# Performance work log

Measured on AMD Instinct MI355X. Metric: run time of the kernel, lower is better.

## Reference

```python
import jax, jax.numpy as jnp
import numpy as np

THRESH = 1.0        # cif_weight_threshold
MAX_HIST = 10       # max_history
RELU_THRESH = 1.0   # relu_threshold (crelu clip)
NORM_SCALAR = 1.0   # normalize_scalar


def setup_inputs() -> dict:
    key = jax.random.key(0)
    k0, k1, k2 = jax.random.split(key, 3)
    B, T, H = 32, 2048, 256
    encoder_outputs = jax.random.normal(k0, (B, T, H), jnp.float32)
    mask = jnp.ones((B, 200, 1), jnp.float32)
    W1 = jax.random.normal(k1, (2 * H, 2 * H), jnp.float32) * 0.02
    b1 = jnp.zeros((2 * H,), jnp.float32)
    W2 = jax.random.normal(k2, (1, 2 * H), jnp.float32) * 0.02
    b2 = jnp.zeros((1,), jnp.float32)
    return {"encoder_outputs": encoder_outputs, "mask": mask,
            "W1": W1, "b1": b1, "W2": W2, "b2": b2, "is_training": 1}


def _cif_forward(x, mask, W1, b1, W2, b2, is_training):
    B, T, H = x.shape
    dt = x.dtype
    # number of non-zero (effective) frames per utterance
    first_pad = jnp.sum((jnp.sum(jnp.abs(x), -1) != 0.0).astype(jnp.int32), 1)  # [B]

    # ---- history chunk: mean over window [max(0, t-MAX_HIST), t); t==0 uses x[:,0] ----
    cs = jnp.concatenate([jnp.zeros((B, 1, H), dt), jnp.cumsum(x, axis=1)], axis=1)  # [B,T+1,H]
    t_idx = jnp.arange(T)
    start = jnp.maximum(0, t_idx - MAX_HIST)
    count = jnp.maximum(t_idx - start, 1).astype(dt)
    hist = (cs[:, t_idx, :] - cs[:, start, :]) / count[None, :, None]     # [B,T,H]
    hist = jnp.where((t_idx == 0)[None, :, None], x[:, 0:1, :], hist)

    # ---- weight prediction (two dense layers, crelu + clip) ----
    info = jnp.concatenate([x, x - hist], axis=-1)                        # [B,T,2H]
    h = jnp.einsum('btc,oc->bto', info, W1) + b1
    w = (jnp.einsum('btc,oc->bto', h, W2) + b2)[..., 0]                   # [B,T]
    w = jnp.clip(jax.nn.relu(w), None, RELU_THRESH)
    ori_weight = w
    sum_a = w.sum(1)

    if is_training:  # static python int; using_scaling=True, mask provided
        N = mask[:, :, 0].sum(-1) - 1.0
        scale = N / jnp.clip(sum_a, 1e-8)
        scale = jnp.where(sum_a == 0, jnp.zeros_like(sum_a), scale)
        w = scale[:, None] * w

    pad_mask = t_idx[None, :] > first_pad[:, None]                        # [B,T]
    w = jnp.where(pad_mask, 0.0, w)

    # ---- accumulate-and-fire scan ----
    def step(carry, inp):
        prev_w, prev_s = carry
        w_t, x_t = inp                                                    # [B], [B,H]
        fired = prev_w + w_t > THRESH
        remained = THRESH - prev_w
        new_w = jnp.where(fired, w_t - remained, w_t + prev_w)
        integ = prev_s + (1.0 - w_t)[:, None] * x_t
        new_s = jnp.where(fired[:, None], x_t, integ)
        fired_s = jnp.where(fired[:, None], integ, jnp.zeros_like(integ))
        return (new_w, new_s), (fired, fired_s)

    init = (jnp.zeros((B,), dt), x[:, 0, :])
    (fin_w, fin_s), (fired_flags, fired_states) = jax.lax.scan(
        step, init, (w.T, jnp.swapaxes(x, 0, 1)))

    fired_states = jnp.swapaxes(fired_states, 0, 1)                       # [B,T,H]
    fired_flag = fired_flags.T[:, :, None].astype(dt)                     # [B,T,1]
    fired_states = jnp.where(pad_mask[:, :, None], 0.0, fired_states)
    fired_states = jnp.concatenate([fired_states, fin_s[:, None, :]], 1)  # [B,T+1,H] (tail)

    # ---- compact fired states to the front (torch truncates to max fired len;
    #      here we keep fixed length T+1 and pad with zeros, which is a superset) ----
    L = T + 1
    fired_marks = (jnp.sum(jnp.abs(fired_states), -1) != 0.0).astype(jnp.int32)
    pos = jnp.cumsum(fired_marks, axis=1) - 1
    pos = jnp.where(fired_marks == 1, pos, L)  # out-of-bounds -> dropped
    cif = jnp.zeros((B, L, H), dt)
    cif = cif.at[jnp.arange(B)[:, None], pos].set(fired_states, mode='drop')

    not_padding_after_cif = (jnp.sum(jnp.abs(cif), -1) != 0.0).astype(jnp.int32)
    norm = jnp.linalg.norm(cif, axis=-1, keepdims=True)
    cif = NORM_SCALAR * cif / jnp.maximum(norm, 1e-12)  # F.normalize(p=2)
    return cif, ori_weight, fired_flag, not_padding_after_cif, sum_a


def reference(encoder_outputs, mask, W1, b1, W2, b2, is_training):
    return _cif_forward(encoder_outputs, mask, W1, b1, W2, b2, is_training)
```

## Files before the change

kernel.cpp:

```cpp
#include <hip/hip_runtime.h>

#define B_ 32
#define T_ 2048
#define H_ 256
#define L_ 2049

__device__ inline double waveReduceD(double v) {
#pragma unroll
  for (int off = 32; off > 0; off >>= 1) v += __shfl_xor(v, off, 64);
  return v;
}

typedef float vfloat4 __attribute__((ext_vector_type(4)));
__device__ inline void nt_store4(float4 v, float* p) {
  vfloat4 t;
  t.x = v.x; t.y = v.y; t.z = v.z; t.w = v.w;
  __builtin_nontemporal_store(t, (vfloat4*)p);
}

__global__ void __launch_bounds__(256) k0_fold(
    const float* __restrict__ W1, const float* __restrict__ b1,
    const float* __restrict__ W2, const float* __restrict__ b2,
    double* __restrict__ vd, double* __restrict__ c0) {
  __shared__ double s_p[8][32];
  int tid = threadIdx.x;
  int cl = tid & 31, sl = tid >> 5;
  int c = blockIdx.x * 32 + cl;
  double acc0 = 0.0, acc1 = 0.0;
#pragma unroll 4
  for (int o = sl * 64; o < sl * 64 + 64; o += 2) {
    acc0 += (double)W2[o] * (double)W1[o * 512 + c];
    acc1 += (double)W2[o + 1] * (double)W1[(o + 1) * 512 + c];
  }
  s_p[sl][cl] = acc0 + acc1;
  __syncthreads();
  if (sl == 0) {
    double v = 0.0;
#pragma unroll
    for (int i = 0; i < 8; ++i) v += s_p[i][cl];
    vd[c] = v;
  }
  if (blockIdx.x == 0) {
    __shared__ double red[256];
    double p = (double)W2[tid] * (double)b1[tid] +
               (double)W2[tid + 256] * (double)b1[tid + 256];
    red[tid] = p;
    __syncthreads();
    for (int s = 128; s > 0; s >>= 1) {
      if (tid < s) red[tid] += red[tid + s];
      __syncthreads();
    }
    if (tid == 0) c0[0] = red[0] + (double)b2[0];
  }
}

__global__ void __launch_bounds__(256) k1_rowdots(
    const float* __restrict__ x, const double* __restrict__ vd,
    double* __restrict__ d1, double* __restrict__ d2, float* __restrict__ absS) {
  int tid = threadIdx.x;
  int s = tid & 15;
  int slot = tid >> 4;
  long rowBase = (long)blockIdx.x * 64;

  double v12[16], v2v[16];
#pragma unroll
  for (int k = 0; k < 16; ++k) {
    double bv = vd[256 + s * 16 + k];
    v2v[k] = bv;
    v12[k] = vd[s * 16 + k] + bv;
  }

#pragma unroll
  for (int i = 0; i < 4; ++i) {
    long row = rowBase + slot * 4 + i;
    const float4* xr = (const float4*)(x + row * H_ + s * 16);
    float4 a0 = xr[0], a1 = xr[1], a2 = xr[2], a3 = xr[3];
    float e[16];
    *(float4*)(e + 0) = a0; *(float4*)(e + 4) = a1;
    *(float4*)(e + 8) = a2; *(float4*)(e + 12) = a3;
    double p1 = 0.0, p2 = 0.0;
    bool nz = false;
#pragma unroll
    for (int k = 0; k < 16; ++k) {
      p1 += (double)e[k] * v12[k];
      p2 += (double)e[k] * v2v[k];
      nz |= (e[k] != 0.0f);
    }
    float nzf = nz ? 1.0f : 0.0f;
#pragma unroll
    for (int off = 1; off < 16; off <<= 1) {
      p1 += __shfl_xor(p1, off, 64);
      p2 += __shfl_xor(p2, off, 64);
      nzf += __shfl_xor(nzf, off, 64);
    }
    if (s == 0) {
      d1[row] = p1;
      d2[row] = p2;
      absS[row] = (nzf > 0.0f) ? 1.0f : 0.0f;
    }
  }
}

__global__ void __launch_bounds__(256) k2_weights(
    const double* __restrict__ d1, const double* __restrict__ d2,
    const float* __restrict__ absS, const float* __restrict__ mask,
    const int* __restrict__ is_tr, const double* __restrict__ c0p,
    float* __restrict__ o_ori, float* __restrict__ o_sa, float* __restrict__ o_ff,
    float* __restrict__ wsc, int* __restrict__ fireT,
    int* __restrict__ nAllArr, int* __restrict__ nUnmArr) {
  __shared__ double s_P[T_];
  __shared__ double s_tot[4];
  __shared__ double s_red[4][3];
  __shared__ double s_tot2[4];
  __shared__ double s_mtot[4];
  __shared__ int s_int[2];
  int b = blockIdx.x, tid = threadIdx.x;
  int lane = tid & 63, wv = tid >> 6;
  int t0 = tid * 8;
  const double* d1b = d1 + (long)b * T_;
  const double* d2b = d2 + (long)b * T_;
  const float* asb = absS + (long)b * T_;
  double c0 = c0p[0];

  double r2[8];
  {
    double run2 = 0.0;
#pragma unroll
    for (int k = 0; k < 8; ++k) { run2 += d2b[t0 + k]; r2[k] = run2; }
    double sc2 = run2;
#pragma unroll
    for (int off = 1; off < 64; off <<= 1) {
      double n = __shfl_up(sc2, off, 64);
      if (lane >= off) sc2 += n;
    }
    if (lane == 63) s_tot[wv] = sc2;
    __syncthreads();
    double base2 = 0.0;
    for (int i = 0; i < wv; ++i) base2 += s_tot[i];
    double e2 = base2 + (sc2 - run2);
#pragma unroll
    for (int k = 0; k < 8; ++k) s_P[t0 + k] = e2 + r2[k];
  }
  __syncthreads();

  double wd[8];
  double sa = 0.0, fpc = 0.0;
#pragma unroll
  for (int k = 0; k < 8; ++k) {
    int t = t0 + k;
    double wvv;
    if (t == 0) {
      wvv = d1b[0] - s_P[0] + c0;
    } else {
      int start = t - 10; if (start < 0) start = 0;
      double ws_ = s_P[t - 1] - (start > 0 ? s_P[start - 1] : 0.0);
      wvv = d1b[t] - ws_ / (double)(t - start) + c0;
    }
    wvv = wvv < 0.0 ? 0.0 : (wvv > 1.0 ? 1.0 : wvv);
    wd[k] = wvv;
    sa += wvv;
    fpc += (asb[t] != 0.0f) ? 1.0 : 0.0;
  }
  {
    float4* ov = (float4*)(o_ori + (long)b * T_ + t0);
    ov[0] = make_float4((float)wd[0], (float)wd[1], (float)wd[2], (float)wd[3]);
    ov[1] = make_float4((float)wd[4], (float)wd[5], (float)wd[6], (float)wd[7]);
  }
  double ms = (tid < 200) ? (double)mask[(long)b * 200 + tid] : 0.0;
  double sar = waveReduceD(sa), fpr = waveReduceD(fpc), msr = waveReduceD(ms);
  if (lane == 0) { s_red[wv][0] = sar; s_red[wv][1] = fpr; s_red[wv][2] = msr; }
  __syncthreads();
  double sumA = s_red[0][0] + s_red[1][0] + s_red[2][0] + s_red[3][0];
  double fpD  = s_red[0][1] + s_red[1][1] + s_red[2][1] + s_red[3][1];
  double maskSum = s_red[0][2] + s_red[1][2] + s_red[2][2] + s_red[3][2];
  if (tid == 0) o_sa[b] = (float)sumA;
  int firstPad = (int)(fpD + 0.5);
  double scale;
  if (is_tr[0] != 0) {
    scale = (sumA == 0.0) ? 0.0 : (maskSum - 1.0) / (sumA > 1e-8 ? sumA : 1e-8);
  } else {
    scale = 1.0;
  }

  double a[8], r[8];
  double run = 0.0;
#pragma unroll
  for (int k = 0; k < 8; ++k) {
    int t = t0 + k;
    double av = wd[k] * scale;
    if (t > firstPad) av = 0.0;
    a[k] = av;
    run += av; r[k] = run;
  }
  {
    float4* wvv = (float4*)(wsc + (long)b * T_ + t0);
    wvv[0] = make_float4((float)a[0], (float)a[1], (float)a[2], (float)a[3]);
    wvv[1] = make_float4((float)a[4], (float)a[5], (float)a[6], (float)a[7]);
  }
  double sc = run;
#pragma unroll
  for (int off = 1; off < 64; off <<= 1) {
    double n = __shfl_up(sc, off, 64);
    if (lane >= off) sc += n;
  }
  if (lane == 63) s_tot2[wv] = sc;
  __syncthreads();
  double base = 0.0;
  for (int i = 0; i < wv; ++i) base += s_tot2[i];
  double e = base + (sc - run);

  double m[8];
  double mn = 1e300;
#pragma unroll
  for (int k = 0; k < 8; ++k) {
    double S = e + r[k];
    double kp = ceil(S - 1.0); if (kp < 0.0) kp = 0.0;
    double D = kp - (double)(t0 + k);
    mn = fmin(mn, D);
    m[k] = mn;
  }
  double scm = mn;
#pragma unroll
  for (int off = 1; off < 64; off <<= 1) {
    double n = __shfl_up(scm, off, 64);
    if (lane >= off) scm = fmin(scm, n);
  }
  double exw = __shfl_up(scm, 1, 64);
  if (lane == 0) exw = 1e300;
  if (lane == 63) s_mtot[wv] = scm;
  __syncthreads();
  double mbase = 1e300;
  for (int i = 0; i < wv; ++i) mbase = fmin(mbase, s_mtot[i]);
  double Mexcl = fmin(mbase, exw);

  float flags[8];
  int Cp = (t0 - 1) + (int)fmin(1.0, Mexcl);
#pragma unroll
  for (int k = 0; k < 8; ++k) {
    int t = t0 + k;
    double Mk = fmin(Mexcl, m[k]);
    int C = t + (int)fmin(1.0, Mk);
    bool fired = C > Cp;
    flags[k] = fired ? 1.0f : 0.0f;
    if (fired) fireT[(long)b * T_ + (C - 1)] = t;
    if (t == firstPad) s_int[0] = C;
    Cp = C;
  }
  {
    float4* fv = (float4*)(o_ff + (long)b * T_ + t0);
    fv[0] = make_float4(flags[0], flags[1], flags[2], flags[3]);
    fv[1] = make_float4(flags[4], flags[5], flags[6], flags[7]);
  }
  if (tid == 255) s_int[1] = Cp;
  __syncthreads();
  if (tid == 0) {
    int nA = s_int[1];
    nAllArr[b] = nA;
    nUnmArr[b] = (firstPad >= T_) ? nA : s_int[0];
  }
}

__global__ void __launch_bounds__(256) k4_rows(
    const float* __restrict__ x, const float* __restrict__ wsc,
    const int* __restrict__ fireT,
    const int* __restrict__ nAllArr, const int* __restrict__ nUnmArr,
    float* __restrict__ cif, float* __restrict__ notpad) {
  int wave = threadIdx.x >> 6, lane = threadIdx.x & 63;
  int pos = blockIdx.x * 4 + wave;
  int b = blockIdx.y;
  if (pos >= L_) return;
  int nA = nAllArr[b], nU = nUnmArr[b];
  float* crow = cif + ((long)b * L_ + pos) * H_ + lane * 4;
  if (pos > nU) {
    nt_store4(make_float4(0.0f, 0.0f, 0.0f, 0.0f), crow);
    if (lane == 0) notpad[(long)b * L_ + pos] = 0.0f;
    return;
  }
  const int* ftb = fireT + (long)b * T_;
  int hi, anchor, lo;
  if (pos < nU) {
    hi = ftb[pos];
    anchor = (pos == 0) ? 0 : ftb[pos - 1];
    lo = (pos == 0) ? 0 : anchor + 1;
  } else {
    hi = T_ - 1;
    anchor = (nA == 0) ? 0 : ftb[nA - 1];
    lo = (nA == 0) ? 0 : anchor + 1;
  }
  const float* xb = x + (long)b * T_ * H_;
  float4 acc = ((const float4*)(xb + (long)anchor * H_))[lane];
  float4 acc2 = make_float4(0.0f, 0.0f, 0.0f, 0.0f);
  const float* wb = wsc + (long)b * T_;
  int u = lo;
  for (; u + 1 <= hi; u += 2) {
    float f0 = 1.0f - wb[u];
    float f1 = 1.0f - wb[u + 1];
    float4 xv0 = ((const float4*)(xb + (long)u * H_))[lane];
    float4 xv1 = ((const float4*)(xb + (long)(u + 1) * H_))[lane];
    acc.x += f0 * xv0.x;  acc.y += f0 * xv0.y;
    acc.z += f0 * xv0.z;  acc.w += f0 * xv0.w;
    acc2.x += f1 * xv1.x; acc2.y += f1 * xv1.y;
    acc2.z += f1 * xv1.z; acc2.w += f1 * xv1.w;
  }
  if (u <= hi) {
    float f = 1.0f - wb[u];
    float4 xv = ((const float4*)(xb + (long)u * H_))[lane];
    acc.x += f * xv.x; acc.y += f * xv.y; acc.z += f * xv.z; acc.w += f * xv.w;
  }
  acc.x += acc2.x; acc.y += acc2.y; acc.z += acc2.z; acc.w += acc2.w;
  float ss = acc.x * acc.x + acc.y * acc.y + acc.z * acc.z + acc.w * acc.w;
#pragma unroll
  for (int off = 32; off > 0; off >>= 1) ss += __shfl_xor(ss, off, 64);
  float inv = 1.0f / fmaxf(sqrtf(ss), 1e-12f);
  nt_store4(make_float4(acc.x * inv, acc.y * inv, acc.z * inv, acc.w * inv), crow);
  if (lane == 0) notpad[(long)b * L_ + pos] = 1.0f;
}

extern "C" void kernel_launch(void* const* d_in, const int* in_sizes, int n_in,
                              void* d_out, int out_size, void* d_ws, size_t ws_size,
                              hipStream_t stream) {
  const float* x    = (const float*)d_in[0];
  const float* mask = (const float*)d_in[1];
  const float* W1   = (const float*)d_in[2];
  const float* b1   = (const float*)d_in[3];
  const float* W2   = (const float*)d_in[4];
  const float* b2   = (const float*)d_in[5];
  const int*   istr = (const int*)d_in[6];

  float* out = (float*)d_out;
  float* o_cif = out;
  float* o_ori = o_cif + (size_t)B_ * L_ * H_;
  float* o_ff  = o_ori + (size_t)B_ * T_;
  float* o_np  = o_ff  + (size_t)B_ * T_;
  float* o_sa  = o_np  + (size_t)B_ * L_;

  char* w = (char*)d_ws;
  double* vd   = (double*)w; w += 512 * 8;
  double* c0   = (double*)w; w += 8;
  double* d1   = (double*)w; w += (size_t)B_ * T_ * 8;
  double* d2   = (double*)w; w += (size_t)B_ * T_ * 8;
  float* absS  = (float*)w;  w += (size_t)B_ * T_ * 4;
  float* wsc   = (float*)w;  w += (size_t)B_ * T_ * 4;
  int* fireT   = (int*)w;    w += (size_t)B_ * T_ * 4;
  int* nAllA   = (int*)w;    w += B_ * 4;
  int* nUnmA   = (int*)w;    w += B_ * 4;

  k0_fold<<<16, 256, 0, stream>>>(W1, b1, W2, b2, vd, c0);
  k1_rowdots<<<(B_ * T_) / 64, 256, 0, stream>>>(x, vd, d1, d2, absS);
  k2_weights<<<B_, 256, 0, stream>>>(d1, d2, absS, mask, istr, c0,
                                     o_ori, o_sa, o_ff, wsc, fireT,
                                     nAllA, nUnmA);
  k4_rows<<<dim3((L_ + 3) / 4, B_), 256, 0, stream>>>(
      x, wsc, fireT, nAllA, nUnmA, o_cif, o_np);
}
```

Before: 153.1 us.

## Fuse four CIF kernels into one cooperative persistent kernel with grid syncs

```diff
diff --git a/kernel.cpp b/kernel.cpp
--- a/kernel.cpp
+++ b/kernel.cpp
@@ -1,4 +1,7 @@
 #include <hip/hip_runtime.h>
+#include <hip/hip_cooperative_groups.h>
+
+namespace cg = cooperative_groups;
 
 #define B_ 32
 #define T_ 2048
@@ -18,302 +21,307 @@
   __builtin_nontemporal_store(t, (vfloat4*)p);
 }
 
-__global__ void __launch_bounds__(256) k0_fold(
+__global__ void __launch_bounds__(256, 2) cif_fused(
+    const float* __restrict__ x, const float* __restrict__ mask,
     const float* __restrict__ W1, const float* __restrict__ b1,
     const float* __restrict__ W2, const float* __restrict__ b2,
-    double* __restrict__ vd, double* __restrict__ c0) {
-  __shared__ double s_p[8][32];
-  int tid = threadIdx.x;
-  int cl = tid & 31, sl = tid >> 5;
-  int c = blockIdx.x * 32 + cl;
-  double acc0 = 0.0, acc1 = 0.0;
-#pragma unroll 4
-  for (int o = sl * 64; o < sl * 64 + 64; o += 2) {
-    acc0 += (double)W2[o] * (double)W1[o * 512 + c];
-    acc1 += (double)W2[o + 1] * (double)W1[(o + 1) * 512 + c];
-  }
-  s_p[sl][cl] = acc0 + acc1;
-  __syncthreads();
-  if (sl == 0) {
-    double v = 0.0;
-#pragma unroll
-    for (int i = 0; i < 8; ++i) v += s_p[i][cl];
-    vd[c] = v;
-  }
-  if (blockIdx.x == 0) {
-    __shared__ double red[256];
-    double p = (double)W2[tid] * (double)b1[tid] +
-               (double)W2[tid + 256] * (double)b1[tid + 256];
-    red[tid] = p;
-    __syncthreads();
-    for (int s = 128; s > 0; s >>= 1) {
-      if (tid < s) red[tid] += red[tid + s];
-      __syncthreads();
-    }
-    if (tid == 0) c0[0] = red[0] + (double)b2[0];
-  }
-}
-
-__global__ void __launch_bounds__(256) k1_rowdots(
-    const float* __restrict__ x, const double* __restrict__ vd,
-    double* __restrict__ d1, double* __restrict__ d2, float* __restrict__ absS) {
-  int tid = threadIdx.x;
-  int s = tid & 15;
-  int slot = tid >> 4;
-  long rowBase = (long)blockIdx.x * 64;
-
-  double v12[16], v2v[16];
-#pragma unroll
-  for (int k = 0; k < 16; ++k) {
-    double bv = vd[256 + s * 16 + k];
-    v2v[k] = bv;
-    v12[k] = vd[s * 16 + k] + bv;
-  }
-
-#pragma unroll
-  for (int i = 0; i < 4; ++i) {
-    long row = rowBase + slot * 4 + i;
-    const float4* xr = (const float4*)(x + row * H_ + s * 16);
-    float4 a0 = xr[0], a1 = xr[1], a2 = xr[2], a3 = xr[3];
-    float e[16];
-    *(float4*)(e + 0) = a0; *(float4*)(e + 4) = a1;
-    *(float4*)(e + 8) = a2; *(float4*)(e + 12) = a3;
-    double p1 = 0.0, p2 = 0.0;
-    bool nz = false;
-#pragma unroll
-    for (int k = 0; k < 16; ++k) {
-      p1 += (double)e[k] * v12[k];
-      p2 += (double)e[k] * v2v[k];
-      nz |= (e[k] != 0.0f);
-    }
-    float nzf = nz ? 1.0f : 0.0f;
-#pragma unroll
-    for (int off = 1; off < 16; off <<= 1) {
-      p1 += __shfl_xor(p1, off, 64);
-      p2 += __shfl_xor(p2, off, 64);
-      nzf += __shfl_xor(nzf, off, 64);
-    }
-    if (s == 0) {
-      d1[row] = p1;
-      d2[row] = p2;
-      absS[row] = (nzf > 0.0f) ? 1.0f : 0.0f;
-    }
-  }
-}
-
-__global__ void __launch_bounds__(256) k2_weights(
-    const double* __restrict__ d1, const double* __restrict__ d2,
-    const float* __restrict__ absS, const float* __restrict__ mask,
-    const int* __restrict__ is_tr, const double* __restrict__ c0p,
-    float* __restrict__ o_ori, float* __restrict__ o_sa, float* __restrict__ o_ff,
-    float* __restrict__ wsc, int* __restrict__ fireT,
-    int* __restrict__ nAllArr, int* __restrict__ nUnmArr) {
+    const int* __restrict__ is_tr,
+    double* __restrict__ vd, double* __restrict__ c0p,
+    double* __restrict__ d1, double* __restrict__ d2,
+    float* __restrict__ absS, float* __restrict__ wsc,
+    int* __restrict__ fireT, int* __restrict__ nAllArr, int* __restrict__ nUnmArr,
+    float* __restrict__ o_cif, float* __restrict__ o_ori,
+    float* __restrict__ o_ff, float* __restrict__ o_np, float* __restrict__ o_sa) {
+  cg::grid_group grid = cg::this_grid();
   __shared__ double s_P[T_];
   __shared__ double s_tot[4];
   __shared__ double s_red[4][3];
   __shared__ double s_tot2[4];
   __shared__ double s_mtot[4];
   __shared__ int s_int[2];
-  int b = blockIdx.x, tid = threadIdx.x;
-  int lane = tid & 63, wv = tid >> 6;
-  int t0 = tid * 8;
-  const double* d1b = d1 + (long)b * T_;
-  const double* d2b = d2 + (long)b * T_;
-  const float* asb = absS + (long)b * T_;
-  double c0 = c0p[0];
-
-  double r2[8];
+  int tid = threadIdx.x;
+
+  if (blockIdx.x < 16) {
+    double (*s_p)[32] = (double(*)[32])s_P;
+    double* red = s_P + 256;
+    int cl = tid & 31, sl = tid >> 5;
+    int c = blockIdx.x * 32 + cl;
+    double acc0 = 0.0, acc1 = 0.0;
+#pragma unroll 4
+    for (int o = sl * 64; o < sl * 64 + 64; o += 2) {
+      acc0 += (double)W2[o] * (double)W1[o * 512 + c];
+      acc1 += (double)W2[o + 1] * (double)W1[(o + 1) * 512 + c];
+    }
+    s_p[sl][cl] = acc0 + acc1;
+    __syncthreads();
+    if (sl == 0) {
+      double v = 0.0;
+#pragma unroll
+      for (int i = 0; i < 8; ++i) v += s_p[i][cl];
+      vd[c] = v;
+    }
+    if (blockIdx.x == 0) {
+      __syncthreads();
+      red[tid] = (double)W2[tid] * (double)b1[tid] +
+                 (double)W2[tid + 256] * (double)b1[tid + 256];
+      __syncthreads();
+      for (int s = 128; s > 0; s >>= 1) {
+        if (tid < s) red[tid] += red[tid + s];
+        __syncthreads();
+      }
+      if (tid == 0) c0p[0] = red[0] + (double)b2[0];
+    }
+  }
+  grid.sync();
+
   {
-    double run2 = 0.0;
-#pragma unroll
-    for (int k = 0; k < 8; ++k) { run2 += d2b[t0 + k]; r2[k] = run2; }
-    double sc2 = run2;
+    int s = tid & 15;
+    int slot = tid >> 4;
+    double v12[16], v2v[16];
+#pragma unroll
+    for (int k = 0; k < 16; ++k) {
+      double bv = vd[256 + s * 16 + k];
+      v2v[k] = bv;
+      v12[k] = vd[s * 16 + k] + bv;
+    }
+#pragma unroll
+    for (int g = 0; g < 2; ++g) {
+      long rowBase = (long)blockIdx.x * 128 + g * 64;
+#pragma unroll
+      for (int i = 0; i < 4; ++i) {
+        long row = rowBase + slot * 4 + i;
+        const float4* xr = (const float4*)(x + row * H_ + s * 16);
+        float4 a0 = xr[0], a1 = xr[1], a2 = xr[2], a3 = xr[3];
+        float e[16];
+        *(float4*)(e + 0) = a0; *(float4*)(e + 4) = a1;
+        *(float4*)(e + 8) = a2; *(float4*)(e + 12) = a3;
+        double p1 = 0.0, p2 = 0.0;
+        bool nz = false;
+#pragma unroll
+        for (int k = 0; k < 16; ++k) {
+          p1 += (double)e[k] * v12[k];
+          p2 += (double)e[k] * v2v[k];
+          nz |= (e[k] != 0.0f);
+        }
+        float nzf = nz ? 1.0f : 0.0f;
+#pragma unroll
+        for (int off = 1; off < 16; off <<= 1) {
+          p1 += __shfl_xor(p1, off, 64);
+          p2 += __shfl_xor(p2, off, 64);
+          nzf += __shfl_xor(nzf, off, 64);
+        }
+        if (s == 0) {
+          d1[row] = p1;
+          d2[row] = p2;
+          absS[row] = (nzf > 0.0f) ? 1.0f : 0.0f;
+        }
+      }
+    }
+  }
+  grid.sync();
+
+  if (blockIdx.x < 32) {
+    int b = blockIdx.x;
+    int lane = tid & 63, wv = tid >> 6;
+    int t0 = tid * 8;
+    const double* d1b = d1 + (long)b * T_;
+    const double* d2b = d2 + (long)b * T_;
+    const float* asb = absS + (long)b * T_;
+    double c0 = c0p[0];
+
+    double r2[8];
+    {
+      double run2 = 0.0;
+#pragma unroll
+      for (int k = 0; k < 8; ++k) { run2 += d2b[t0 + k]; r2[k] = run2; }
+      double sc2 = run2;
+#pragma unroll
+      for (int off = 1; off < 64; off <<= 1) {
+        double n = __shfl_up(sc2, off, 64);
+        if (lane >= off) sc2 += n;
+      }
+      if (lane == 63) s_tot[wv] = sc2;
+      __syncthreads();
+      double base2 = 0.0;
+      for (int i = 0; i < wv; ++i) base2 += s_tot[i];
+      double e2 = base2 + (sc2 - run2);
+#pragma unroll
+      for (int k = 0; k < 8; ++k) s_P[t0 + k] = e2 + r2[k];
+    }
+    __syncthreads();
+
+    double wd[8];
+    double sa = 0.0, fpc = 0.0;
+#pragma unroll
+    for (int k = 0; k < 8; ++k) {
+      int t = t0 + k;
+      double wvv;
+      if (t == 0) {
+        wvv = d1b[0] - s_P[0] + c0;
+      } else {
+        int start = t - 10; if (start < 0) start = 0;
+        double ws_ = s_P[t - 1] - (start > 0 ? s_P[start - 1] : 0.0);
+        wvv = d1b[t] - ws_ / (double)(t - start) + c0;
+      }
+      wvv = wvv < 0.0 ? 0.0 : (wvv > 1.0 ? 1.0 : wvv);
+      wd[k] = wvv;
+      sa += wvv;
+      fpc += (asb[t] != 0.0f) ? 1.0 : 0.0;
+    }
+    {
+      float4* ov = (float4*)(o_ori + (long)b * T_ + t0);
+      ov[0] = make_float4((float)wd[0], (float)wd[1], (float)wd[2], (float)wd[3]);
+      ov[1] = make_float4((float)wd[4], (float)wd[5], (float)wd[6], (float)wd[7]);
+    }
+    double ms = (tid < 200) ? (double)mask[(long)b * 200 + tid] : 0.0;
+    double sar = waveReduceD(sa), fpr = waveReduceD(fpc), msr = waveReduceD(ms);
+    if (lane == 0) { s_red[wv][0] = sar; s_red[wv][1] = fpr; s_red[wv][2] = msr; }
+    __syncthreads();
+    double sumA = s_red[0][0] + s_red[1][0] + s_red[2][0] + s_red[3][0];
+    double fpD  = s_red[0][1] + s_red[1][1] + s_red[2][1] + s_red[3][1];
+    double maskSum = s_red[0][2] + s_red[1][2] + s_red[2][2] + s_red[3][2];
+    if (tid == 0) o_sa[b] = (float)sumA;
+    int firstPad = (int)(fpD + 0.5);
+    double scale;
+    if (is_tr[0] != 0) {
+      scale = (sumA == 0.0) ? 0.0 : (maskSum - 1.0) / (sumA > 1e-8 ? sumA : 1e-8);
+    } else {
+      scale = 1.0;
+    }
+
+    double a[8], r[8];
+    double run = 0.0;
+#pragma unroll
+    for (int k = 0; k < 8; ++k) {
+      int t = t0 + k;
+      double av = wd[k] * scale;
+      if (t > firstPad) av = 0.0;
+      a[k] = av;
+      run += av; r[k] = run;
+    }
+    {
+      float4* wvv = (float4*)(wsc + (long)b * T_ + t0);
+      wvv[0] = make_float4((float)a[0], (float)a[1], (float)a[2], (float)a[3]);
+      wvv[1] = make_float4((float)a[4], (float)a[5], (float)a[6], (float)a[7]);
+    }
+    double sc = run;
 #pragma unroll
     for (int off = 1; off < 64; off <<= 1) {
-      double n = __shfl_up(sc2, off, 64);
-      if (lane >= off) sc2 += n;
-    }
-    if (lane == 63) s_tot[wv] = sc2;
-    __syncthreads();
-    double base2 = 0.0;
-    for (int i = 0; i < wv; ++i) base2 += s_tot[i];
-    double e2 = base2 + (sc2 - run2);
-#pragma unroll
-    for (int k = 0; k < 8; ++k) s_P[t0 + k] = e2 + r2[k];
+      double n = __shfl_up(sc, off, 64);
+      if (lane >= off) sc += n;
+    }
+    if (lane == 63) s_tot2[wv] = sc;
+    __syncthreads();
+    double base = 0.0;
+    for (int i = 0; i < wv; ++i) base += s_tot2[i];
+    double e = base + (sc - run);
+
+    double m[8];
+    double mn = 1e300;
+#pragma unroll
+    for (int k = 0; k < 8; ++k) {
+      double S = e + r[k];
+      double kp = ceil(S - 1.0); if (kp < 0.0) kp = 0.0;
+      double D = kp - (double)(t0 + k);
+      mn = fmin(mn, D);
+      m[k] = mn;
+    }
+    double scm = mn;
+#pragma unroll
+    for (int off = 1; off < 64; off <<= 1) {
+      double n = __shfl_up(scm, off, 64);
+      if (lane >= off) scm = fmin(scm, n);
+    }
+    double exw = __shfl_up(scm, 1, 64);
+    if (lane == 0) exw = 1e300;
+    if (lane == 63) s_mtot[wv] = scm;
+    __syncthreads();
+    double mbase = 1e300;
+    for (int i = 0; i < wv; ++i) mbase = fmin(mbase, s_mtot[i]);
+    double Mexcl = fmin(mbase, exw);
+
+    float flags[8];
+    int Cp = (t0 - 1) + (int)fmin(1.0, Mexcl);
+#pragma unroll
+    for (int k = 0; k < 8; ++k) {
+      int t = t0 + k;
+      double Mk = fmin(Mexcl, m[k]);
+      int C = t + (int)fmin(1.0, Mk);
+      bool fired = C > Cp;
+      flags[k] = fired ? 1.0f : 0.0f;
+      if (fired) fireT[(long)b * T_ + (C - 1)] = t;
+      if (t == firstPad) s_int[0] = C;
+      Cp = C;
+    }
+    {
+      float4* fv = (float4*)(o_ff + (long)b * T_ + t0);
+      fv[0] = make_float4(flags[0], flags[1], flags[2], flags[3]);
+      fv[1] = make_float4(flags[4], flags[5], flags[6], flags[7]);
+    }
+    if (tid == 255) s_int[1] = Cp;
+    __syncthreads();
+    if (tid == 0) {
+      int nA = s_int[1];
+      nAllArr[b] = nA;
+      nUnmArr[b] = (firstPad >= T_) ? nA : s_int[0];
+    }
   }
-  __syncthreads();
-
-  double wd[8];
-  double sa = 0.0, fpc = 0.0;
-#pragma unroll
-  for (int k = 0; k < 8; ++k) {
-    int t = t0 + k;
-    double wvv;
-    if (t == 0) {
-      wvv = d1b[0] - s_P[0] + c0;
-    } else {
-      int start = t - 10; if (start < 0) start = 0;
-      double ws_ = s_P[t - 1] - (start > 0 ? s_P[start - 1] : 0.0);
-      wvv = d1b[t] - ws_ / (double)(t - start) + c0;
-    }
-    wvv = wvv < 0.0 ? 0.0 : (wvv > 1.0 ? 1.0 : wvv);
-    wd[k] = wvv;
-    sa += wvv;
-    fpc += (asb[t] != 0.0f) ? 1.0 : 0.0;
+  grid.sync();
+
+  {
+    int lane = tid & 63;
+    int waveId = blockIdx.x * 4 + (tid >> 6);
+    const int nWaves = 512 * 4;
+    for (int task = waveId; task < B_ * L_; task += nWaves) {
+      int b = task / L_;
+      int pos = task - b * L_;
+      int nA = nAllArr[b], nU = nUnmArr[b];
+      float* crow = o_cif + ((long)b * L_ + pos) * H_ + lane * 4;
+      if (pos > nU) {
+        nt_store4(make_float4(0.0f, 0.0f, 0.0f, 0.0f), crow);
+        if (lane == 0) o_np[(long)b * L_ + pos] = 0.0f;
+        continue;
+      }
+      const int* ftb = fireT + (long)b * T_;
+      int hi, anchor, lo;
+      if (pos < nU) {
+        hi = ftb[pos];
+        anchor = (pos == 0) ? 0 : ftb[pos - 1];
+        lo = (pos == 0) ? 0 : anchor + 1;
+      } else {
+        hi = T_ - 1;
+        anchor = (nA == 0) ? 0 : ftb[nA - 1];
+        lo = (nA == 0) ? 0 : anchor + 1;
+      }
+      const float* xb = x + (long)b * T_ * H_;
+      float4 acc = ((const float4*)(xb + (long)anchor * H_))[lane];
+      float4 acc2 = make_float4(0.0f, 0.0f, 0.0f, 0.0f);
+      const float* wb = wsc + (long)b * T_;
+      int u = lo;
+      for (; u + 1 <= hi; u += 2) {
+        float f0 = 1.0f - wb[u];
+        float f1 = 1.0f - wb[u + 1];
+        float4 xv0 = ((const float4*)(xb + (long)u * H_))[lane];
+        float4 xv1 = ((const float4*)(xb + (long)(u + 1) * H_))[lane];
+        acc.x += f0 * xv0.x;  acc.y += f0 * xv0.y;
+        acc.z += f0 * xv0.z;  acc.w += f0 * xv0.w;
+        acc2.x += f1 * xv1.x; acc2.y += f1 * xv1.y;
+        acc2.z += f1 * xv1.z; acc2.w += f1 * xv1.w;
+      }
+      if (u <= hi) {
+        float f = 1.0f - wb[u];
+        float4 xv = ((const float4*)(xb + (long)u * H_))[lane];
+        acc.x += f * xv.x; acc.y += f * xv.y; acc.z += f * xv.z; acc.w += f * xv.w;
+      }
+      acc.x += acc2.x; acc.y += acc2.y; acc.z += acc2.z; acc.w += acc2.w;
+      float ss = acc.x * acc.x + acc.y * acc.y + acc.z * acc.z + acc.w * acc.w;
+#pragma unroll
+      for (int off = 32; off > 0; off >>= 1) ss += __shfl_xor(ss, off, 64);
+      float inv = 1.0f / fmaxf(sqrtf(ss), 1e-12f);
+      nt_store4(make_float4(acc.x * inv, acc.y * inv, acc.z * inv, acc.w * inv), crow);
+      if (lane == 0) o_np[(long)b * L_ + pos] = 1.0f;
+    }
   }
-  {
-    float4* ov = (float4*)(o_ori + (long)b * T_ + t0);
-    ov[0] = make_float4((float)wd[0], (float)wd[1], (float)wd[2], (float)wd[3]);
-    ov[1] = make_float4((float)wd[4], (float)wd[5], (float)wd[6], (float)wd[7]);
-  }
-  double ms = (tid < 200) ? (double)mask[(long)b * 200 + tid] : 0.0;
-  double sar = waveReduceD(sa), fpr = waveReduceD(fpc), msr = waveReduceD(ms);
-  if (lane == 0) { s_red[wv][0] = sar; s_red[wv][1] = fpr; s_red[wv][2] = msr; }
-  __syncthreads();
-  double sumA = s_red[0][0] + s_red[1][0] + s_red[2][0] + s_red[3][0];
-  double fpD  = s_red[0][1] + s_red[1][1] + s_red[2][1] + s_red[3][1];
-  double maskSum = s_red[0][2] + s_red[1][2] + s_red[2][2] + s_red[3][2];
-  if (tid == 0) o_sa[b] = (float)sumA;
-  int firstPad = (int)(fpD + 0.5);
-  double scale;
-  if (is_tr[0] != 0) {
-    scale = (sumA == 0.0) ? 0.0 : (maskSum - 1.0) / (sumA > 1e-8 ? sumA : 1e-8);
-  } else {
-    scale = 1.0;
-  }
-
-  double a[8], r[8];
-  double run = 0.0;
-#pragma unroll
-  for (int k = 0; k < 8; ++k) {
-    int t = t0 + k;
-    double av = wd[k] * scale;
-    if (t > firstPad) av = 0.0;
-    a[k] = av;
-    run += av; r[k] = run;
-  }
-  {
-    float4* wvv = (float4*)(wsc + (long)b * T_ + t0);
-    wvv[0] = make_float4((float)a[0], (float)a[1], (float)a[2], (float)a[3]);
-    wvv[1] = make_float4((float)a[4], (float)a[5], (float)a[6], (float)a[7]);
-  }
-  double sc = run;
-#pragma unroll
-  for (int off = 1; off < 64; off <<= 1) {
-    double n = __shfl_up(sc, off, 64);
-    if (lane >= off) sc += n;
-  }
-  if (lane == 63) s_tot2[wv] = sc;
-  __syncthreads();
-  double base = 0.0;
-  for (int i = 0; i < wv; ++i) base += s_tot2[i];
-  double e = base + (sc - run);
-
-  double m[8];
-  double mn = 1e300;
-#pragma unroll
-  for (int k = 0; k < 8; ++k) {
-    double S = e + r[k];
-    double kp = ceil(S - 1.0); if (kp < 0.0) kp = 0.0;
-    double D = kp - (double)(t0 + k);
-    mn = fmin(mn, D);
-    m[k] = mn;
-  }
-  double scm = mn;
-#pragma unroll
-  for (int off = 1; off < 64; off <<= 1) {
-    double n = __shfl_up(scm, off, 64);
-    if (lane >= off) scm = fmin(scm, n);
-  }
-  double exw = __shfl_up(scm, 1, 64);
-  if (lane == 0) exw = 1e300;
-  if (lane == 63) s_mtot[wv] = scm;
-  __syncthreads();
-  double mbase = 1e300;
-  for (int i = 0; i < wv; ++i) mbase = fmin(mbase, s_mtot[i]);
-  double Mexcl = fmin(mbase, exw);
-
-  float flags[8];
-  int Cp = (t0 - 1) + (int)fmin(1.0, Mexcl);
-#pragma unroll
-  for (int k = 0; k < 8; ++k) {
-    int t = t0 + k;
-    double Mk = fmin(Mexcl, m[k]);
-    int C = t + (int)fmin(1.0, Mk);
-    bool fired = C > Cp;
-    flags[k] = fired ? 1.0f : 0.0f;
-    if (fired) fireT[(long)b * T_ + (C - 1)] = t;
-    if (t == firstPad) s_int[0] = C;
-    Cp = C;
-  }
-  {
-    float4* fv = (float4*)(o_ff + (long)b * T_ + t0);
-    fv[0] = make_float4(flags[0], flags[1], flags[2], flags[3]);
-    fv[1] = make_float4(flags[4], flags[5], flags[6], flags[7]);
-  }
-  if (tid == 255) s_int[1] = Cp;
-  __syncthreads();
-  if (tid == 0) {
-    int nA = s_int[1];
-    nAllArr[b] = nA;
-    nUnmArr[b] = (firstPad >= T_) ? nA : s_int[0];
-  }
-}
-
-__global__ void __launch_bounds__(256) k4_rows(
-    const float* __restrict__ x, const float* __restrict__ wsc,
-    const int* __restrict__ fireT,
-    const int* __restrict__ nAllArr, const int* __restrict__ nUnmArr,
-    float* __restrict__ cif, float* __restrict__ notpad) {
-  int wave = threadIdx.x >> 6, lane = threadIdx.x & 63;
-  int pos = blockIdx.x * 4 + wave;
-  int b = blockIdx.y;
-  if (pos >= L_) return;
-  int nA = nAllArr[b], nU = nUnmArr[b];
-  float* crow = cif + ((long)b * L_ + pos) * H_ + lane * 4;
-  if (pos > nU) {
-    nt_store4(make_float4(0.0f, 0.0f, 0.0f, 0.0f), crow);
-    if (lane == 0) notpad[(long)b * L_ + pos] = 0.0f;
-    return;
-  }
-  const int* ftb = fireT + (long)b * T_;
-  int hi, anchor, lo;
-  if (pos < nU) {
-    hi = ftb[pos];
-    anchor = (pos == 0) ? 0 : ftb[pos - 1];
-    lo = (pos == 0) ? 0 : anchor + 1;
-  } else {
-    hi = T_ - 1;
-    anchor = (nA == 0) ? 0 : ftb[nA - 1];
-    lo = (nA == 0) ? 0 : anchor + 1;
-  }
-  const float* xb = x + (long)b * T_ * H_;
-  float4 acc = ((const float4*)(xb + (long)anchor * H_))[lane];
-  float4 acc2 = make_float4(0.0f, 0.0f, 0.0f, 0.0f);
-  const float* wb = wsc + (long)b * T_;
-  int u = lo;
-  for (; u + 1 <= hi; u += 2) {
-    float f0 = 1.0f - wb[u];
-    float f1 = 1.0f - wb[u + 1];
-    float4 xv0 = ((const float4*)(xb + (long)u * H_))[lane];
-    float4 xv1 = ((const float4*)(xb + (long)(u + 1) * H_))[lane];
-    acc.x += f0 * xv0.x;  acc.y += f0 * xv0.y;
-    acc.z += f0 * xv0.z;  acc.w += f0 * xv0.w;
-    acc2.x += f1 * xv1.x; acc2.y += f1 * xv1.y;
-    acc2.z += f1 * xv1.z; acc2.w += f1 * xv1.w;
-  }
-  if (u <= hi) {
-    float f = 1.0f - wb[u];
-    float4 xv = ((const float4*)(xb + (long)u * H_))[lane];
-    acc.x += f * xv.x; acc.y += f * xv.y; acc.z += f * xv.z; acc.w += f * xv.w;
-  }
-  acc.x += acc2.x; acc.y += acc2.y; acc.z += acc2.z; acc.w += acc2.w;
-  float ss = acc.x * acc.x + acc.y * acc.y + acc.z * acc.z + acc.w * acc.w;
-#pragma unroll
-  for (int off = 32; off > 0; off >>= 1) ss += __shfl_xor(ss, off, 64);
-  float inv = 1.0f / fmaxf(sqrtf(ss), 1e-12f);
-  nt_store4(make_float4(acc.x * inv, acc.y * inv, acc.z * inv, acc.w * inv), crow);
-  if (lane == 0) notpad[(long)b * L_ + pos] = 1.0f;
 }
 
 extern "C" void kernel_launch(void* const* d_in, const int* in_sizes, int n_in,
@@ -345,11 +353,11 @@
   int* nAllA   = (int*)w;    w += B_ * 4;
   int* nUnmA   = (int*)w;    w += B_ * 4;
 
-  k0_fold<<<16, 256, 0, stream>>>(W1, b1, W2, b2, vd, c0);
-  k1_rowdots<<<(B_ * T_) / 64, 256, 0, stream>>>(x, vd, d1, d2, absS);
-  k2_weights<<<B_, 256, 0, stream>>>(d1, d2, absS, mask, istr, c0,
-                                     o_ori, o_sa, o_ff, wsc, fireT,
-                                     nAllA, nUnmA);
-  k4_rows<<<dim3((L_ + 3) / 4, B_), 256, 0, stream>>>(
-      x, wsc, fireT, nAllA, nUnmA, o_cif, o_np);
+  void* args[] = {
+    (void*)&x, (void*)&mask, (void*)&W1, (void*)&b1, (void*)&W2, (void*)&b2,
+    (void*)&istr, (void*)&vd, (void*)&c0, (void*)&d1, (void*)&d2, (void*)&absS,
+    (void*)&wsc, (void*)&fireT, (void*)&nAllA, (void*)&nUnmA,
+    (void*)&o_cif, (void*)&o_ori, (void*)&o_ff, (void*)&o_np, (void*)&o_sa
+  };
+  hipLaunchCooperativeKernel(cif_fused, dim3(512), dim3(256), args, 0, stream);
 }
```

Result: slower. 389.0 us (+154.1%).

## Fuse weight/scan kernel into row-accumulation kernel with redundant per-block scan

Applied to the files above, without the earlier changes.

```diff
diff --git a/kernel.cpp b/kernel.cpp
--- a/kernel.cpp
+++ b/kernel.cpp
@@ -101,20 +101,24 @@
   }
 }
 
-__global__ void __launch_bounds__(256) k2_weights(
+__global__ void __launch_bounds__(256) k24_rows(
+    const float* __restrict__ x, const float* __restrict__ mask,
+    const int* __restrict__ is_tr, const double* __restrict__ c0p,
     const double* __restrict__ d1, const double* __restrict__ d2,
-    const float* __restrict__ absS, const float* __restrict__ mask,
-    const int* __restrict__ is_tr, const double* __restrict__ c0p,
-    float* __restrict__ o_ori, float* __restrict__ o_sa, float* __restrict__ o_ff,
-    float* __restrict__ wsc, int* __restrict__ fireT,
-    int* __restrict__ nAllArr, int* __restrict__ nUnmArr) {
+    const float* __restrict__ absS,
+    float* __restrict__ o_cif, float* __restrict__ o_ori,
+    float* __restrict__ o_ff, float* __restrict__ o_np,
+    float* __restrict__ o_sa) {
   __shared__ double s_P[T_];
+  __shared__ float s_wf[T_];
+  __shared__ int s_fireT[T_];
   __shared__ double s_tot[4];
   __shared__ double s_red[4][3];
   __shared__ double s_tot2[4];
   __shared__ double s_mtot[4];
   __shared__ int s_int[2];
-  int b = blockIdx.x, tid = threadIdx.x;
+  int pg = blockIdx.x, b = blockIdx.y;
+  int tid = threadIdx.x;
   int lane = tid & 63, wv = tid >> 6;
   int t0 = tid * 8;
   const double* d1b = d1 + (long)b * T_;
@@ -161,7 +165,7 @@
     sa += wvv;
     fpc += (asb[t] != 0.0f) ? 1.0 : 0.0;
   }
-  {
+  if (pg == 0) {
     float4* ov = (float4*)(o_ori + (long)b * T_ + t0);
     ov[0] = make_float4((float)wd[0], (float)wd[1], (float)wd[2], (float)wd[3]);
     ov[1] = make_float4((float)wd[4], (float)wd[5], (float)wd[6], (float)wd[7]);
@@ -173,7 +177,7 @@
   double sumA = s_red[0][0] + s_red[1][0] + s_red[2][0] + s_red[3][0];
   double fpD  = s_red[0][1] + s_red[1][1] + s_red[2][1] + s_red[3][1];
   double maskSum = s_red[0][2] + s_red[1][2] + s_red[2][2] + s_red[3][2];
-  if (tid == 0) o_sa[b] = (float)sumA;
+  if (pg == 0 && tid == 0) o_sa[b] = (float)sumA;
   int firstPad = (int)(fpD + 0.5);
   double scale;
   if (is_tr[0] != 0) {
@@ -191,11 +195,7 @@
     if (t > firstPad) av = 0.0;
     a[k] = av;
     run += av; r[k] = run;
-  }
-  {
-    float4* wvv = (float4*)(wsc + (long)b * T_ + t0);
-    wvv[0] = make_float4((float)a[0], (float)a[1], (float)a[2], (float)a[3]);
-    wvv[1] = make_float4((float)a[4], (float)a[5], (float)a[6], (float)a[7]);
+    s_wf[t] = (float)av;
   }
   double sc = run;
 #pragma unroll
@@ -242,78 +242,66 @@
     int C = t + (int)fmin(1.0, Mk);
     bool fired = C > Cp;
     flags[k] = fired ? 1.0f : 0.0f;
-    if (fired) fireT[(long)b * T_ + (C - 1)] = t;
+    if (fired) s_fireT[C - 1] = t;
     if (t == firstPad) s_int[0] = C;
     Cp = C;
   }
-  {
+  if (pg == 0) {
     float4* fv = (float4*)(o_ff + (long)b * T_ + t0);
     fv[0] = make_float4(flags[0], flags[1], flags[2], flags[3]);
     fv[1] = make_float4(flags[4], flags[5], flags[6], flags[7]);
   }
   if (tid == 255) s_int[1] = Cp;
   __syncthreads();
-  if (tid == 0) {
-    int nA = s_int[1];
-    nAllArr[b] = nA;
-    nUnmArr[b] = (firstPad >= T_) ? nA : s_int[0];
-  }
-}
-
-__global__ void __launch_bounds__(256) k4_rows(
-    const float* __restrict__ x, const float* __restrict__ wsc,
-    const int* __restrict__ fireT,
-    const int* __restrict__ nAllArr, const int* __restrict__ nUnmArr,
-    float* __restrict__ cif, float* __restrict__ notpad) {
-  int wave = threadIdx.x >> 6, lane = threadIdx.x & 63;
-  int pos = blockIdx.x * 4 + wave;
-  int b = blockIdx.y;
-  if (pos >= L_) return;
-  int nA = nAllArr[b], nU = nUnmArr[b];
-  float* crow = cif + ((long)b * L_ + pos) * H_ + lane * 4;
-  if (pos > nU) {
-    nt_store4(make_float4(0.0f, 0.0f, 0.0f, 0.0f), crow);
-    if (lane == 0) notpad[(long)b * L_ + pos] = 0.0f;
-    return;
-  }
-  const int* ftb = fireT + (long)b * T_;
-  int hi, anchor, lo;
-  if (pos < nU) {
-    hi = ftb[pos];
-    anchor = (pos == 0) ? 0 : ftb[pos - 1];
-    lo = (pos == 0) ? 0 : anchor + 1;
-  } else {
-    hi = T_ - 1;
-    anchor = (nA == 0) ? 0 : ftb[nA - 1];
-    lo = (nA == 0) ? 0 : anchor + 1;
-  }
+  int nA = s_int[1];
+  int nU = (firstPad >= T_) ? nA : s_int[0];
+
+  int wave = wv;
   const float* xb = x + (long)b * T_ * H_;
-  float4 acc = ((const float4*)(xb + (long)anchor * H_))[lane];
-  float4 acc2 = make_float4(0.0f, 0.0f, 0.0f, 0.0f);
-  const float* wb = wsc + (long)b * T_;
-  int u = lo;
-  for (; u + 1 <= hi; u += 2) {
-    float f0 = 1.0f - wb[u];
-    float f1 = 1.0f - wb[u + 1];
-    float4 xv0 = ((const float4*)(xb + (long)u * H_))[lane];
-    float4 xv1 = ((const float4*)(xb + (long)(u + 1) * H_))[lane];
-    acc.x += f0 * xv0.x;  acc.y += f0 * xv0.y;
-    acc.z += f0 * xv0.z;  acc.w += f0 * xv0.w;
-    acc2.x += f1 * xv1.x; acc2.y += f1 * xv1.y;
-    acc2.z += f1 * xv1.z; acc2.w += f1 * xv1.w;
-  }
-  if (u <= hi) {
-    float f = 1.0f - wb[u];
-    float4 xv = ((const float4*)(xb + (long)u * H_))[lane];
-    acc.x += f * xv.x; acc.y += f * xv.y; acc.z += f * xv.z; acc.w += f * xv.w;
-  }
-  acc.x += acc2.x; acc.y += acc2.y; acc.z += acc2.z; acc.w += acc2.w;
-  float ss = acc.x * acc.x + acc.y * acc.y + acc.z * acc.z + acc.w * acc.w;
-#pragma unroll
-  for (int off = 32; off > 0; off >>= 1) ss += __shfl_xor(ss, off, 64);
-  float inv = 1.0f / fmaxf(sqrtf(ss), 1e-12f);
-  nt_store4(make_float4(acc.x * inv, acc.y * inv, acc.z * inv, acc.w * inv), crow);
-  if (lane == 0) notpad[(long)b * L_ + pos] = 1.0f;
+  for (int idx = wave; pg + 32 * idx < L_; idx += 4) {
+    int pos = pg + 32 * idx;
+    float* crow = o_cif + ((long)b * L_ + pos) * H_ + lane * 4;
+    if (pos > nU) {
+      nt_store4(make_float4(0.0f, 0.0f, 0.0f, 0.0f), crow);
+      if (lane == 0) o_np[(long)b * L_ + pos] = 0.0f;
+      continue;
+    }
+    int hi, anchor, lo;
+    if (pos < nU) {
+      hi = s_fireT[pos];
+      anchor = (pos == 0) ? 0 : s_fireT[pos - 1];
+      lo = (pos == 0) ? 0 : anchor + 1;
+    } else {
+      hi = T_ - 1;
+      anchor = (nA == 0) ? 0 : s_fireT[nA - 1];
+      lo = (nA == 0) ? 0 : anchor + 1;
+    }
+    float4 acc = ((const float4*)(xb + (long)anchor * H_))[lane];
+    float4 acc2 = make_float4(0.0f, 0.0f, 0.0f, 0.0f);
+    int u = lo;
+    for (; u + 1 <= hi; u += 2) {
+      float f0 = 1.0f - s_wf[u];
+      float f1 = 1.0f - s_wf[u + 1];
+      float4 xv0 = ((const float4*)(xb + (long)u * H_))[lane];
+      float4 xv1 = ((const float4*)(xb + (long)(u + 1) * H_))[lane];
+      acc.x += f0 * xv0.x;  acc.y += f0 * xv0.y;
+      acc.z += f0 * xv0.z;  acc.w += f0 * xv0.w;
+      acc2.x += f1 * xv1.x; acc2.y += f1 * xv1.y;
+      acc2.z += f1 * xv1.z; acc2.w += f1 * xv1.w;
+    }
+    if (u <= hi) {
+      float f = 1.0f - s_wf[u];
+      float4 xv = ((const float4*)(xb + (long)u * H_))[lane];
+      acc.x += f * xv.x; acc.y += f * xv.y; acc.z += f * xv.z; acc.w += f * xv.w;
+    }
+    acc.x += acc2.x; acc.y += acc2.y; acc.z += acc2.z; acc.w += acc2.w;
+    float ss = acc.x * acc.x + acc.y * acc.y + acc.z * acc.z + acc.w * acc.w;
+#pragma unroll
+    for (int off = 32; off > 0; off >>= 1) ss += __shfl_xor(ss, off, 64);
+    float inv = 1.0f / fmaxf(sqrtf(ss), 1e-12f);
+    nt_store4(make_float4(acc.x * inv, acc.y * inv, acc.z * inv, acc.w * inv), crow);
+    if (lane == 0) o_np[(long)b * L_ + pos] = 1.0f;
+  }
 }
 
 extern "C" void kernel_launch(void* const* d_in, const int* in_sizes, int n_in,
@@ -340,16 +328,9 @@
   double* d1   = (double*)w; w += (size_t)B_ * T_ * 8;
   double* d2   = (double*)w; w += (size_t)B_ * T_ * 8;
   float* absS  = (float*)w;  w += (size_t)B_ * T_ * 4;
-  float* wsc   = (float*)w;  w += (size_t)B_ * T_ * 4;
-  int* fireT   = (int*)w;    w += (size_t)B_ * T_ * 4;
-  int* nAllA   = (int*)w;    w += B_ * 4;
-  int* nUnmA   = (int*)w;    w += B_ * 4;
 
   k0_fold<<<16, 256, 0, stream>>>(W1, b1, W2, b2, vd, c0);
   k1_rowdots<<<(B_ * T_) / 64, 256, 0, stream>>>(x, vd, d1, d2, absS);
-  k2_weights<<<B_, 256, 0, stream>>>(d1, d2, absS, mask, istr, c0,
-                                     o_ori, o_sa, o_ff, wsc, fireT,
-                                     nAllA, nUnmA);
-  k4_rows<<<dim3((L_ + 3) / 4, B_), 256, 0, stream>>>(
-      x, wsc, fireT, nAllA, nUnmA, o_cif, o_np);
-}
+  k24_rows<<<dim3(32, B_), 256, 0, stream>>>(x, mask, istr, c0, d1, d2, absS,
+                                             o_cif, o_ori, o_ff, o_np, o_sa);
+}
```

Measured after the change: 154.3 us. Within noise of the previous version (+0.8%).
